# Optimization experiments

Measured on AMD Instinct MI355X. Metric: run time of the kernel, lower is better.

Reference implementation:

```python
import jax, jax.numpy as jnp
import numpy as np

D_MODEL = 1024
K = 256
AMPLITUDE_MAX = 3.0
GATE_BIAS_INIT = 0.65  # alpha-gate bias initialized at logit(0.65)


def setup_inputs() -> dict:
    key = jax.random.key(0)
    k0, k1, k2, k3 = jax.random.split(key, 4)
    B, n = 4, 4096
    x = jax.random.normal(k0, (B, n, D_MODEL), dtype=jnp.float32)
    # OscillatorProjection: Linear(d_model -> 6K), chunks [A, omega, phi, alpha, g, beta]
    W_proj = jax.random.normal(k1, (6 * K, D_MODEL), dtype=jnp.float32) * 0.02
    b_proj = jnp.zeros((6 * K,), dtype=jnp.float32)
    alpha_bias = float(np.log(GATE_BIAS_INIT / (1.0 - GATE_BIAS_INIT)))
    b_proj = b_proj.at[3 * K:4 * K].set(alpha_bias)
    W_res = jax.random.normal(k2, (D_MODEL, 4 * K - 2), dtype=jnp.float32) * 0.002
    W_phase = jax.random.normal(k3, (K, D_MODEL), dtype=jnp.float32) * 0.001
    b_phase = jnp.zeros((K,), dtype=jnp.float32)
    return {
        "x": x, "W_proj": W_proj, "b_proj": b_proj, "W_res": W_res,
        "W_phase": W_phase, "b_phase": b_phase,
        "lambda_pcg": jnp.float32(0.1), "res_scale": jnp.float32(0.05),
    }


def _scan_combine(c1, c2):
    # first-order linear recurrence r_t = a_t * r_{t-1} + b_t (complex, split re/im)
    a1, br1, bi1 = c1
    a2, br2, bi2 = c2
    return (a1 * a2, a2 * br1 + br2, a2 * bi1 + bi2)


def _forward(x, W_proj, b_proj, W_res, W_phase, b_phase, lambda_pcg, res_scale):
    B, n, _ = x.shape
    # OscillatorProjection
    proj = jnp.einsum('bnd,kd->bnk', x, W_proj) + b_proj  # (B, n, 6K)
    a_raw, w_raw, p_raw, al_raw, g_raw, be_raw = jnp.split(proj, 6, axis=-1)
    A = AMPLITUDE_MAX * jax.nn.sigmoid(a_raw)
    omega = jax.nn.softplus(w_raw)
    phi = p_raw
    alpha = jax.nn.sigmoid(al_raw)
    g_out = jax.nn.sigmoid(g_raw)
    beta = jax.nn.sigmoid(be_raw)

    # phase_mode == 'log'
    positions = jnp.log1p(jnp.arange(n, dtype=jnp.float32)).reshape(1, n, 1)
    angle = omega * positions + phi
    cos_a = jnp.cos(angle)
    sin_a = jnp.sin(angle)
    one_m_a = 1.0 - alpha
    drive_r = one_m_a * A * cos_a
    drive_i = one_m_a * A * sin_a

    # parallel associative prefix scan over sequence axis
    _, r_r, r_i = jax.lax.associative_scan(_scan_combine, (alpha, drive_r, drive_i), axis=1)

    # erase (read-and-subtract)
    readout = r_r * cos_a + r_i * sin_a
    r_r = r_r - beta * readout * cos_a
    r_i = r_i - beta * readout * sin_a

    # state norm: r /= max(|r|, 1)
    modulus = jnp.sqrt(r_r * r_r + r_i * r_i + 1e-8)
    scale = jnp.maximum(modulus, 1.0)
    r_r = r_r / scale
    r_i = r_i / scale

    # demodulate: rho = r * exp(-j * angle)
    rho_re = r_r * cos_a + r_i * sin_a
    rho_im = -r_r * sin_a + r_i * cos_a

    # phase-coherence gate
    rho_norm = jnp.sqrt(rho_re * rho_re + rho_im * rho_im + 1e-8)
    phase_query = jnp.einsum('bnd,kd->bnk', x, W_phase) + b_phase
    phase_alignment = (rho_re / rho_norm) * jnp.cos(phase_query) + (rho_im / rho_norm) * jnp.sin(phase_query)
    phase_gate = jax.nn.sigmoid(lambda_pcg * phase_alignment)
    rho_re = phase_gate * rho_re
    rho_im = phase_gate * rho_im

    # SCPM: neighbor complex cross-products
    xcross_re = rho_re[:, :, :-1] * rho_re[:, :, 1:] - rho_im[:, :, :-1] * rho_im[:, :, 1:]
    xcross_im = rho_re[:, :, :-1] * rho_im[:, :, 1:] + rho_im[:, :, :-1] * rho_re[:, :, 1:]
    rho_base = jnp.concatenate([rho_re, rho_im], axis=-1)              # (B, n, 2K)
    g_base = jnp.concatenate([g_out, g_out], axis=-1)
    g_cross = 0.5 * (g_out[:, :, :-1] + g_out[:, :, 1:])
    xcross = jnp.concatenate([xcross_re, xcross_im], axis=-1)          # (B, n, 2K-2)
    g_cross_full = jnp.concatenate([g_cross, g_cross], axis=-1)
    rho = jnp.concatenate([g_base * rho_base, g_cross_full * xcross], axis=-1)  # (B, n, 4K-2)

    # eval mode: warmup_factor == 1.0
    return res_scale * jnp.einsum('bnk,dk->bnd', rho, W_res)


def reference(x, W_proj, b_proj, W_res, W_phase, b_phase, lambda_pcg, res_scale):
    return _forward(x, W_proj, b_proj, W_res, W_phase, b_phase, lambda_pcg, res_scale)
```

## Files before the change

### kernel.cpp

```cpp
#include <hip/hip_runtime.h>
#include <cmath>

#define D_MODEL 1024
#define KOSC    256
#define NSEQ    4096
#define BATCH   4
#define NROW    (BATCH * NSEQ)
#define JTOT    1792

typedef short      s16x8 __attribute__((ext_vector_type(8)));
typedef float      f32x4 __attribute__((ext_vector_type(4)));

#define GL2LDS(gsrc, ldst)                                                      \
  __builtin_amdgcn_global_load_lds(                                             \
      (const __attribute__((address_space(1))) unsigned int*)(gsrc),            \
      (__attribute__((address_space(3))) unsigned int*)(ldst), 16, 0, 0)

__device__ __forceinline__ float sigm(float x) {
    return 1.0f / (1.0f + expf(-x));
}
__device__ __forceinline__ float softplusf_(float x) {
    return fmaxf(x, 0.0f) + log1pf(expf(-fabsf(x)));
}

__device__ __forceinline__ void bf16_split(float f, unsigned short& hi,
                                           unsigned short& lo) {
    unsigned u = __float_as_uint(f);
    unsigned r = u + 0x7FFFu + ((u >> 16) & 1u);
    hi = (unsigned short)(r >> 16);
    float fh = __uint_as_float((unsigned)hi << 16);
    float fl = f - fh;
    unsigned ul = __float_as_uint(fl);
    unsigned rl = ul + 0x7FFFu + ((ul >> 16) & 1u);
    lo = (unsigned short)(rl >> 16);
}

__global__ __launch_bounds__(256) void split_x_kernel(
    const float* __restrict__ x, unsigned short* __restrict__ XH,
    unsigned short* __restrict__ XL)
{
    int i = blockIdx.x * 256 + threadIdx.x;
    float4 v = ((const float4*)x)[i];
    ushort4 h, l;
    bf16_split(v.x, h.x, l.x);
    bf16_split(v.y, h.y, l.y);
    bf16_split(v.z, h.z, l.z);
    bf16_split(v.w, h.w, l.w);
    ((ushort4*)XH)[i] = h;
    ((ushort4*)XL)[i] = l;
}

__global__ __launch_bounds__(256) void split_w_kernel(
    const float* __restrict__ Wproj, const float* __restrict__ Wphase,
    unsigned short* __restrict__ WH, unsigned short* __restrict__ WL)
{
    int i = blockIdx.x * 256 + threadIdx.x;
    int elem = i << 2;
    int row = elem >> 10;
    int col = elem & 1023;
    const float* src = (row < 1536) ? (Wproj + (size_t)row * 1024 + col)
                                    : (Wphase + (size_t)(row - 1536) * 1024 + col);
    float4 v = *(const float4*)src;
    ushort4 h, l;
    bf16_split(v.x, h.x, l.x);
    bf16_split(v.y, h.y, l.y);
    bf16_split(v.z, h.z, l.z);
    bf16_split(v.w, h.w, l.w);
    ((ushort4*)WH)[i] = h;
    ((ushort4*)WL)[i] = l;
}

__global__ __launch_bounds__(256) void pack_wres_kernel(
    const float* __restrict__ Wres, unsigned short* __restrict__ WPH)
{
    int idx = blockIdx.x * 256 + threadIdx.x;
    int d = idx >> 10;
    int j = idx & 1023;
    float v = (j < 1022) ? Wres[(size_t)d * 1022 + j] : 0.0f;
    unsigned u = __float_as_uint(v);
    unsigned r = u + 0x7FFFu + ((u >> 16) & 1u);
    WPH[idx] = (unsigned short)(r >> 16);
}

__global__ __launch_bounds__(256, 3) void gemm1_full_kernel(
    const unsigned short* __restrict__ WH, const unsigned short* __restrict__ WL,
    const unsigned short* __restrict__ XH, const unsigned short* __restrict__ XL,
    const float* __restrict__ bproj, float* __restrict__ PT)
{
    __shared__ __attribute__((aligned(16))) unsigned short AH[4096];
    __shared__ __attribute__((aligned(16))) unsigned short AL[4096];
    __shared__ __attribute__((aligned(16))) unsigned short BH[4096];
    __shared__ __attribute__((aligned(16))) unsigned short BL[4096];

    const int tid  = threadIdx.x;
    const int lane = tid & 63;
    const int w    = tid >> 6;
    const int wm   = w >> 1, wn = w & 1;
    const int m0   = (blockIdx.y + 2) * 128;
    const int n0   = blockIdx.x * 128;
    const int fr   = lane & 15;
    const int fq   = lane >> 4;

    f32x4 acc[4][4];
    #pragma unroll
    for (int i = 0; i < 4; i++)
        #pragma unroll
        for (int j = 0; j < 4; j++) acc[i][j] = (f32x4){0.f, 0.f, 0.f, 0.f};

    for (int kc = 0; kc < 32; kc++) {
        const int kbase = kc * 32;
        __syncthreads();
        #pragma unroll
        for (int t = 0; t < 2; t++) {
            int G  = w * 128 + t * 64 + lane;
            int gm = G & 127;
            int gq = G >> 7;
            size_t offA = (size_t)(m0 + gm) * 1024 + kbase + gq * 8;
            size_t offB = (size_t)(n0 + gm) * 1024 + kbase + gq * 8;
            int ldsg = (w * 128 + t * 64) * 8;
            GL2LDS(WH + offA, &AH[ldsg]);
            GL2LDS(WL + offA, &AL[ldsg]);
            GL2LDS(XH + offB, &BH[ldsg]);
            GL2LDS(XL + offB, &BL[ldsg]);
        }
        __syncthreads();

        s16x8 ah[4], al[4], bh[4], bl[4];
        #pragma unroll
        for (int f = 0; f < 4; f++) {
            int aoff = (fq * 128 + wm * 64 + f * 16 + fr) * 8;
            int boff = (fq * 128 + wn * 64 + f * 16 + fr) * 8;
            ah[f] = *(const s16x8*)&AH[aoff];
            al[f] = *(const s16x8*)&AL[aoff];
            bh[f] = *(const s16x8*)&BH[boff];
            bl[f] = *(const s16x8*)&BL[boff];
        }
        #pragma unroll
        for (int i = 0; i < 4; i++)
            #pragma unroll
            for (int j = 0; j < 4; j++) {
                acc[i][j] = __builtin_amdgcn_mfma_f32_16x16x32_bf16(ah[i], bh[j], acc[i][j], 0, 0, 0);
                acc[i][j] = __builtin_amdgcn_mfma_f32_16x16x32_bf16(ah[i], bl[j], acc[i][j], 0, 0, 0);
                acc[i][j] = __builtin_amdgcn_mfma_f32_16x16x32_bf16(al[i], bh[j], acc[i][j], 0, 0, 0);
            }
    }

    #pragma unroll
    for (int i = 0; i < 4; i++) {
        int mbase = m0 + wm * 64 + i * 16 + fq * 4;
        #pragma unroll
        for (int j = 0; j < 4; j++) {
            int n = n0 + wn * 64 + j * 16 + fr;
            #pragma unroll
            for (int rg = 0; rg < 4; rg++) {
                int m = mbase + rg;
                PT[(size_t)m * NROW + n] = acc[i][j][rg] + bproj[m];
            }
        }
    }
}

__global__ __launch_bounds__(256, 4) void gemm1_lite_kernel(
    const unsigned short* __restrict__ WH, const unsigned short* __restrict__ XH,
    const float* __restrict__ bproj, const float* __restrict__ bphase,
    float* __restrict__ PT)
{
    __shared__ __attribute__((aligned(16))) unsigned short AH[4096];
    __shared__ __attribute__((aligned(16))) unsigned short BH[4096];

    const int tid  = threadIdx.x;
    const int lane = tid & 63;
    const int w    = tid >> 6;
    const int wm   = w >> 1, wn = w & 1;
    const int yt   = blockIdx.y;
    const int jt   = (yt < 2) ? yt : yt + 4;
    const int m0   = jt * 128;
    const int n0   = blockIdx.x * 128;
    const int fr   = lane & 15;
    const int fq   = lane >> 4;

    f32x4 acc[4][4];
    #pragma unroll
    for (int i = 0; i < 4; i++)
        #pragma unroll
        for (int j = 0; j < 4; j++) acc[i][j] = (f32x4){0.f, 0.f, 0.f, 0.f};

    for (int kc = 0; kc < 32; kc++) {
        const int kbase = kc * 32;
        __syncthreads();
        #pragma unroll
        for (int t = 0; t < 2; t++) {
            int G  = w * 128 + t * 64 + lane;
            int gm = G & 127;
            int gq = G >> 7;
            size_t offA = (size_t)(m0 + gm) * 1024 + kbase + gq * 8;
            size_t offB = (size_t)(n0 + gm) * 1024 + kbase + gq * 8;
            int ldsg = (w * 128 + t * 64) * 8;
            GL2LDS(WH + offA, &AH[ldsg]);
            GL2LDS(XH + offB, &BH[ldsg]);
        }
        __syncthreads();

        s16x8 ah[4], bh[4];
        #pragma unroll
        for (int f = 0; f < 4; f++) {
            int aoff = (fq * 128 + wm * 64 + f * 16 + fr) * 8;
            int boff = (fq * 128 + wn * 64 + f * 16 + fr) * 8;
            ah[f] = *(const s16x8*)&AH[aoff];
            bh[f] = *(const s16x8*)&BH[boff];
        }
        #pragma unroll
        for (int i = 0; i < 4; i++)
            #pragma unroll
            for (int j = 0; j < 4; j++)
                acc[i][j] = __builtin_amdgcn_mfma_f32_16x16x32_bf16(ah[i], bh[j], acc[i][j], 0, 0, 0);
    }

    #pragma unroll
    for (int i = 0; i < 4; i++) {
        int mbase = m0 + wm * 64 + i * 16 + fq * 4;
        #pragma unroll
        for (int j = 0; j < 4; j++) {
            int n = n0 + wn * 64 + j * 16 + fr;
            #pragma unroll
            for (int rg = 0; rg < 4; rg++) {
                int m = mbase + rg;
                float bias = (m < 1536) ? bproj[m] : bphase[m - 1536];
                PT[(size_t)m * NROW + n] = acc[i][j][rg] + bias;
            }
        }
    }
}

__global__ __launch_bounds__(256) void scan_kernel(float* PT,
                                                   const float* lambda_ptr)
{
    const int bx = blockIdx.x;
    const int k = bx & 255;
    const int b = bx >> 8;
    const int t = threadIdx.x;
    const size_t colb = (size_t)b * NSEQ;
    const size_t R = NROW;

    float* rowA  = PT + (size_t)(k)        * R + colb;
    float* rowW  = PT + (size_t)(256 + k)  * R + colb;
    float* rowP  = PT + (size_t)(512 + k)  * R + colb;
    float* rowAl = PT + (size_t)(768 + k)  * R + colb;
    float* rowG  = PT + (size_t)(1024 + k) * R + colb;
    float* rowBe = PT + (size_t)(1280 + k) * R + colb;
    float* rowPq = PT + (size_t)(1536 + k) * R + colb;

    __shared__ float s_al[NSEQ + 256];
    __shared__ float s_rr[NSEQ + 256];
    __shared__ float s_ri[NSEQ + 256];
    __shared__ float s_sa[256], s_sbr[256], s_sbi[256];

    const float lam = *lambda_ptr;

    for (int i = 0; i < 16; i++) {
        int n = i * 256 + t;
        float araw = rowA[n];
        float wraw = rowW[n];
        float praw = rowP[n];
        float alraw = rowAl[n];
        float A     = 3.0f * sigm(araw);
        float alpha = sigm(alraw);
        float omega = softplusf_(wraw);
        float ang   = fmaf(omega, log1pf((float)n), praw);
        float sn, cs;
        sincosf(ang, &sn, &cs);
        float amp = (1.0f - alpha) * A;
        int pidx = n + (n >> 4);
        s_al[pidx] = alpha;
        s_rr[pidx] = amp * cs;
        s_ri[pidx] = amp * sn;
    }
    __syncthreads();

    {
        float ap = 1.0f, br = 0.0f, bi = 0.0f;
        int base = t * 17;
        #pragma unroll
        for (int i = 0; i < 16; i++) {
            float a = s_al[base + i];
            br = fmaf(a, br, s_rr[base + i]);
            bi = fmaf(a, bi, s_ri[base + i]);
            ap *= a;
        }
        s_sa[t] = ap; s_sbr[t] = br; s_sbi[t] = bi;
    }
    __syncthreads();

    for (int off = 1; off < 256; off <<= 1) {
        float a2 = s_sa[t], b2r = s_sbr[t], b2i = s_sbi[t];
        float a1 = 1.0f, b1r = 0.0f, b1i = 0.0f;
        if (t >= off) { a1 = s_sa[t - off]; b1r = s_sbr[t - off]; b1i = s_sbi[t - off]; }
        __syncthreads();
        s_sa[t]  = a1 * a2;
        s_sbr[t] = fmaf(a2, b1r, b2r);
        s_sbi[t] = fmaf(a2, b1i, b2i);
        __syncthreads();
    }

    {
        float cr = 0.0f, ci = 0.0f;
        if (t > 0) { cr = s_sbr[t - 1]; ci = s_sbi[t - 1]; }
        int base = t * 17;
        #pragma unroll
        for (int i = 0; i < 16; i++) {
            float a = s_al[base + i];
            cr = fmaf(a, cr, s_rr[base + i]);
            ci = fmaf(a, ci, s_ri[base + i]);
            s_rr[base + i] = cr;
            s_ri[base + i] = ci;
        }
    }
    __syncthreads();

    for (int i = 0; i < 16; i++) {
        int n = i * 256 + t;
        float wraw = rowW[n];
        float praw = rowP[n];
        float beraw = rowBe[n];
        float graw = rowG[n];
        float pq = rowPq[n];

        float omega = softplusf_(wraw);
        float ang = fmaf(omega, log1pf((float)n), praw);
        float sn, cs;
        sincosf(ang, &sn, &cs);

        int pidx = n + (n >> 4);
        float rr = s_rr[pidx], ri = s_ri[pidx];
        float beta = sigm(beraw);
        float g = sigm(graw);

        float readout = rr * cs + ri * sn;
        rr -= beta * readout * cs;
        ri -= beta * readout * sn;

        float modulus = sqrtf(rr * rr + ri * ri + 1e-8f);
        float scale = fmaxf(modulus, 1.0f);
        rr /= scale; ri /= scale;

        float rho_re = rr * cs + ri * sn;
        float rho_im = -rr * sn + ri * cs;

        float rho_norm = sqrtf(rho_re * rho_re + rho_im * rho_im + 1e-8f);
        float sq, cq;
        sincosf(pq, &sq, &cq);
        float pa = (rho_re * cq + rho_im * sq) / rho_norm;
        float gate = sigm(lam * pa);
        rho_re *= gate;
        rho_im *= gate;

        rowA[n] = rho_re;
        rowW[n] = rho_im;
        rowP[n] = g;
    }
}

__global__ __launch_bounds__(256) void pack_rho_kernel(
    const float* __restrict__ PT, unsigned short* __restrict__ RTH,
    unsigned short* __restrict__ RTL)
{
    __shared__ float s_re[256 * 33];
    __shared__ float s_im[256 * 33];
    __shared__ float s_g [256 * 33];

    const int tid = threadIdx.x;
    const int r0 = blockIdx.x * 32;

    {
        int lr = tid & 31;
        int k0 = tid >> 5;
        for (int it = 0; it < 32; it++) {
            int k = it * 8 + k0;
            size_t go = (size_t)k * NROW + r0 + lr;
            s_re[k * 33 + lr] = PT[go];
            s_im[k * 33 + lr] = PT[(size_t)256 * NROW + go];
            s_g [k * 33 + lr] = PT[(size_t)512 * NROW + go];
        }
    }
    __syncthreads();

    const int r = tid >> 3;
    const int c = tid & 7;
    for (int i = 0; i < 16; i++) {
        int jb = (c + 8 * i) * 8;
        unsigned short h[8], l[8];
        #pragma unroll
        for (int e = 0; e < 8; e++) {
            int j = jb + e;
            float v;
            if (j < 256) {
                v = s_g[j * 33 + r] * s_re[j * 33 + r];
            } else if (j < 512) {
                int k = j - 256;
                v = s_g[k * 33 + r] * s_im[k * 33 + r];
            } else if (j < 767) {
                int k = j - 512;
                float gc = 0.5f * (s_g[k * 33 + r] + s_g[(k + 1) * 33 + r]);
                v = gc * (s_re[k * 33 + r] * s_re[(k + 1) * 33 + r]
                        - s_im[k * 33 + r] * s_im[(k + 1) * 33 + r]);
            } else if (j < 1022) {
                int k = j - 767;
                float gc = 0.5f * (s_g[k * 33 + r] + s_g[(k + 1) * 33 + r]);
                v = gc * (s_re[k * 33 + r] * s_im[(k + 1) * 33 + r]
                        + s_im[k * 33 + r] * s_re[(k + 1) * 33 + r]);
            } else {
                v = 0.0f;
            }
            bf16_split(v, h[e], l[e]);
        }
        size_t off = (size_t)(r0 + r) * 1024 + jb;
        s16x8 hv, lv;
        #pragma unroll
        for (int e = 0; e < 8; e++) { hv[e] = (short)h[e]; lv[e] = (short)l[e]; }
        *(s16x8*)&RTH[off] = hv;
        *(s16x8*)&RTL[off] = lv;
    }
}

__global__ __launch_bounds__(256, 3) void gemm2_kernel(
    const unsigned short* __restrict__ WPH,
    const unsigned short* __restrict__ RTH, const unsigned short* __restrict__ RTL,
    const float* __restrict__ rs_ptr, float* __restrict__ out)
{
    __shared__ __attribute__((aligned(16))) unsigned short AH[4096];
    __shared__ __attribute__((aligned(16))) unsigned short BH[4096];
    __shared__ __attribute__((aligned(16))) unsigned short BL[4096];

    const int tid  = threadIdx.x;
    const int lane = tid & 63;
    const int w    = tid >> 6;
    const int wm   = w >> 1, wn = w & 1;
    const int m0   = blockIdx.y * 128;
    const int n0   = blockIdx.x * 128;
    const int fr   = lane & 15;
    const int fq   = lane >> 4;
    const float rs = *rs_ptr;

    f32x4 acc[4][4];
    #pragma unroll
    for (int i = 0; i < 4; i++)
        #pragma unroll
        for (int j = 0; j < 4; j++) acc[i][j] = (f32x4){0.f, 0.f, 0.f, 0.f};

    for (int kc = 0; kc < 32; kc++) {
        const int kbase = kc * 32;
        __syncthreads();
        #pragma unroll
        for (int t = 0; t < 2; t++) {
            int G  = w * 128 + t * 64 + lane;
            int gm = G & 127;
            int gq = G >> 7;
            size_t offA = (size_t)(m0 + gm) * 1024 + kbase + gq * 8;
            size_t offB = (size_t)(n0 + gm) * 1024 + kbase + gq * 8;
            int ldsg = (w * 128 + t * 64) * 8;
            GL2LDS(WPH + offA, &AH[ldsg]);
            GL2LDS(RTH + offB, &BH[ldsg]);
            GL2LDS(RTL + offB, &BL[ldsg]);
        }
        __syncthreads();

        s16x8 ah[4], bh[4], bl[4];
        #pragma unroll
        for (int f = 0; f < 4; f++) {
            int aoff = (fq * 128 + wm * 64 + f * 16 + fr) * 8;
            int boff = (fq * 128 + wn * 64 + f * 16 + fr) * 8;
            ah[f] = *(const s16x8*)&AH[aoff];
            bh[f] = *(const s16x8*)&BH[boff];
            bl[f] = *(const s16x8*)&BL[boff];
        }
        #pragma unroll
        for (int i = 0; i < 4; i++)
            #pragma unroll
            for (int j = 0; j < 4; j++) {
                acc[i][j] = __builtin_amdgcn_mfma_f32_16x16x32_bf16(ah[i], bh[j], acc[i][j], 0, 0, 0);
                acc[i][j] = __builtin_amdgcn_mfma_f32_16x16x32_bf16(ah[i], bl[j], acc[i][j], 0, 0, 0);
            }
    }

    #pragma unroll
    for (int i = 0; i < 4; i++) {
        int d = m0 + wm * 64 + i * 16 + fq * 4;
        #pragma unroll
        for (int j = 0; j < 4; j++) {
            int n = n0 + wn * 64 + j * 16 + fr;
            float4 v = { rs * acc[i][j][0], rs * acc[i][j][1],
                         rs * acc[i][j][2], rs * acc[i][j][3] };
            *(float4*)&out[(size_t)n * 1024 + d] = v;
        }
    }
}

extern "C" void kernel_launch(void* const* d_in, const int* in_sizes, int n_in,
                              void* d_out, int out_size, void* d_ws, size_t ws_size,
                              hipStream_t stream)
{
    const float* x      = (const float*)d_in[0];
    const float* Wproj  = (const float*)d_in[1];
    const float* bproj  = (const float*)d_in[2];
    const float* Wres   = (const float*)d_in[3];
    const float* Wphase = (const float*)d_in[4];
    const float* bphase = (const float*)d_in[5];
    const float* lam    = (const float*)d_in[6];
    const float* rs     = (const float*)d_in[7];
    float* out = (float*)d_out;

    float* PT = (float*)d_ws;
    unsigned short* WH  = (unsigned short*)((char*)d_ws + (size_t)JTOT * NROW * 4);
    unsigned short* WL  = WH + (size_t)JTOT * 1024;
    unsigned short* RTH = (unsigned short*)(PT + (size_t)768 * NROW);
    unsigned short* RTL = RTH + (size_t)NROW * 1024;
    unsigned short* WPH = (unsigned short*)PT;
    unsigned short* XH  = (unsigned short*)d_out;
    unsigned short* XL  = XH + (size_t)NROW * 1024;

    hipLaunchKernelGGL(split_x_kernel, dim3(NROW * D_MODEL / 1024), dim3(256), 0, stream,
                       x, XH, XL);
    hipLaunchKernelGGL(split_w_kernel, dim3(JTOT * D_MODEL / 1024), dim3(256), 0, stream,
                       Wproj, Wphase, WH, WL);
    hipLaunchKernelGGL(gemm1_full_kernel, dim3(NROW / 128, 4), dim3(256), 0, stream,
                       WH, WL, XH, XL, bproj, PT);
    hipLaunchKernelGGL(gemm1_lite_kernel, dim3(NROW / 128, 10), dim3(256), 0, stream,
                       WH, XH, bproj, bphase, PT);
    hipLaunchKernelGGL(scan_kernel, dim3(BATCH * KOSC), dim3(256), 0, stream,
                       PT, lam);
    hipLaunchKernelGGL(pack_rho_kernel, dim3(NROW / 32), dim3(256), 0, stream,
                       PT, RTH, RTL);
    hipLaunchKernelGGL(pack_wres_kernel, dim3(1024 * 1024 / 256), dim3(256), 0, stream,
                       Wres, WPH);
    hipLaunchKernelGGL(gemm2_kernel, dim3(NROW / 128, 1024 / 128), dim3(256), 0, stream,
                       WPH, RTH, RTL, rs, out);
}
```

Measured before the change: 535.1 us.

## Unify GEMMs into double-buffered 256x256 tile core with merged gemm1 launch

Replaces the 128x128 single-buffered GEMM kernels with a shared templated 256x256-tile core run by 512 threads. The core double-buffers LDS, prefetching the next K chunk while MFMAs run, and raises wave priority during compute. The full-precision and lite gemm1 launches become one kernel that picks the precision path per row tile, and gemm2 uses the same core. The aims are more reuse per tile, hidden global-load latency and fewer launches, at the cost of more registers and LDS per block, lower occupancy, and fewer blocks for the GPU to schedule.

```diff
diff --git a/kernel.cpp b/kernel.cpp
--- a/kernel.cpp
+++ b/kernel.cpp
@@ -82,150 +82,151 @@
     WPH[idx] = (unsigned short)(r >> 16);
 }
 
-__global__ __launch_bounds__(256, 3) void gemm1_full_kernel(
-    const unsigned short* __restrict__ WH, const unsigned short* __restrict__ WL,
-    const unsigned short* __restrict__ XH, const unsigned short* __restrict__ XL,
-    const float* __restrict__ bproj, float* __restrict__ PT)
-{
-    __shared__ __attribute__((aligned(16))) unsigned short AH[4096];
-    __shared__ __attribute__((aligned(16))) unsigned short AL[4096];
-    __shared__ __attribute__((aligned(16))) unsigned short BH[4096];
-    __shared__ __attribute__((aligned(16))) unsigned short BL[4096];
-
+template<int NKS, int HAS_AL, int HAS_BL>
+__device__ __forceinline__ void gemm256_core(
+    const unsigned short* __restrict__ gAH, const unsigned short* __restrict__ gAL,
+    const unsigned short* __restrict__ gBH, const unsigned short* __restrict__ gBL,
+    unsigned short* sAH, unsigned short* sAL,
+    unsigned short* sBH, unsigned short* sBL,
+    int m0, int n0, f32x4 (&acc)[8][4])
+{
     const int tid  = threadIdx.x;
     const int lane = tid & 63;
     const int w    = tid >> 6;
-    const int wm   = w >> 1, wn = w & 1;
-    const int m0   = (blockIdx.y + 2) * 128;
-    const int n0   = blockIdx.x * 128;
+    const int wm   = w >> 2;
+    const int wn   = w & 3;
     const int fr   = lane & 15;
     const int fq   = lane >> 4;
-
-    f32x4 acc[4][4];
+    const int BK   = 32 * NKS;
+    const int BUFS = 256 * BK;
+    const int NKT  = 1024 / BK;
+
+    auto stage = [&](int buf, int kc, int t) {
+        const int G   = t * 512 + tid;
+        const int row = G & 255;
+        const int q   = G >> 8;
+        const size_t ka   = (size_t)kc * BK + q * 8;
+        const size_t offA = (size_t)(m0 + row) * 1024 + ka;
+        const size_t offB = (size_t)(n0 + row) * 1024 + ka;
+        const int ldso = buf * BUFS + (t * 512 + w * 64) * 8;
+        GL2LDS(gAH + offA, &sAH[ldso]);
+        if (HAS_AL) GL2LDS(gAL + offA, &sAL[ldso]);
+        GL2LDS(gBH + offB, &sBH[ldso]);
+        if (HAS_BL) GL2LDS(gBL + offB, &sBL[ldso]);
+    };
+
     #pragma unroll
-    for (int i = 0; i < 4; i++)
+    for (int t = 0; t < 2 * NKS; t++) stage(0, 0, t);
+
+    for (int kc = 0; kc < NKT; kc++) {
+        const int cur   = kc & 1;
+        const int cbase = cur * BUFS;
+        asm volatile("s_waitcnt vmcnt(0)" ::: "memory");
+        __builtin_amdgcn_s_barrier();
+
+        #pragma unroll
+        for (int p = 0; p < 4; p++) {
+            const int qi = p & 1;
+            const int qj = p >> 1;
+
+            s16x8 fah[4][NKS], fal[4][NKS], fbh[2][NKS], fbl[2][NKS];
+            #pragma unroll
+            for (int ii = 0; ii < 4; ii++) {
+                const int i = qi * 4 + ii;
+                #pragma unroll
+                for (int s = 0; s < NKS; s++) {
+                    const int off = cbase +
+                        (((s * 4 + fq) * 256 + wm * 128 + i * 16 + fr) * 8);
+                    fah[ii][s] = *(const s16x8*)&sAH[off];
+                    if (HAS_AL) fal[ii][s] = *(const s16x8*)&sAL[off];
+                }
+            }
+            #pragma unroll
+            for (int jj = 0; jj < 2; jj++) {
+                const int j = qj * 2 + jj;
+                #pragma unroll
+                for (int s = 0; s < NKS; s++) {
+                    const int off = cbase +
+                        (((s * 4 + fq) * 256 + wn * 64 + j * 16 + fr) * 8);
+                    fbh[jj][s] = *(const s16x8*)&sBH[off];
+                    if (HAS_BL) fbl[jj][s] = *(const s16x8*)&sBL[off];
+                }
+            }
+
+            if (p < 2 && kc + 1 < NKT) {
+                #pragma unroll
+                for (int t = 0; t < NKS; t++)
+                    stage(cur ^ 1, kc + 1, p * NKS + t);
+            }
+
+            __builtin_amdgcn_s_barrier();
+            __builtin_amdgcn_s_setprio(1);
+            #pragma unroll
+            for (int ii = 0; ii < 4; ii++) {
+                #pragma unroll
+                for (int jj = 0; jj < 2; jj++) {
+                    const int i = qi * 4 + ii;
+                    const int j = qj * 2 + jj;
+                    #pragma unroll
+                    for (int s = 0; s < NKS; s++) {
+                        acc[i][j] = __builtin_amdgcn_mfma_f32_16x16x32_bf16(
+                            fah[ii][s], fbh[jj][s], acc[i][j], 0, 0, 0);
+                        if (HAS_BL)
+                            acc[i][j] = __builtin_amdgcn_mfma_f32_16x16x32_bf16(
+                                fah[ii][s], fbl[jj][s], acc[i][j], 0, 0, 0);
+                        if (HAS_AL)
+                            acc[i][j] = __builtin_amdgcn_mfma_f32_16x16x32_bf16(
+                                fal[ii][s], fbh[jj][s], acc[i][j], 0, 0, 0);
+                    }
+                }
+            }
+            __builtin_amdgcn_s_setprio(0);
+            if (p < 3) __builtin_amdgcn_s_barrier();
+        }
+    }
+}
+
+__global__ __launch_bounds__(512, 2) void gemm1_kernel(
+    const unsigned short* __restrict__ WH, const unsigned short* __restrict__ WL,
+    const unsigned short* __restrict__ XH, const unsigned short* __restrict__ XL,
+    const float* __restrict__ bproj, const float* __restrict__ bphase,
+    float* __restrict__ PT)
+{
+    __shared__ __attribute__((aligned(16))) unsigned short smem[65536];
+    const int yt = blockIdx.y;
+    const int m0 = yt * 256;
+    const int n0 = blockIdx.x * 256;
+
+    f32x4 acc[8][4];
+    #pragma unroll
+    for (int i = 0; i < 8; i++)
         #pragma unroll
         for (int j = 0; j < 4; j++) acc[i][j] = (f32x4){0.f, 0.f, 0.f, 0.f};
 
-    for (int kc = 0; kc < 32; kc++) {
-        const int kbase = kc * 32;
-        __syncthreads();
-        #pragma unroll
-        for (int t = 0; t < 2; t++) {
-            int G  = w * 128 + t * 64 + lane;
-            int gm = G & 127;
-            int gq = G >> 7;
-            size_t offA = (size_t)(m0 + gm) * 1024 + kbase + gq * 8;
-            size_t offB = (size_t)(n0 + gm) * 1024 + kbase + gq * 8;
-            int ldsg = (w * 128 + t * 64) * 8;
-            GL2LDS(WH + offA, &AH[ldsg]);
-            GL2LDS(WL + offA, &AL[ldsg]);
-            GL2LDS(XH + offB, &BH[ldsg]);
-            GL2LDS(XL + offB, &BL[ldsg]);
-        }
-        __syncthreads();
-
-        s16x8 ah[4], al[4], bh[4], bl[4];
-        #pragma unroll
-        for (int f = 0; f < 4; f++) {
-            int aoff = (fq * 128 + wm * 64 + f * 16 + fr) * 8;
-            int boff = (fq * 128 + wn * 64 + f * 16 + fr) * 8;
-            ah[f] = *(const s16x8*)&AH[aoff];
-            al[f] = *(const s16x8*)&AL[aoff];
-            bh[f] = *(const s16x8*)&BH[boff];
-            bl[f] = *(const s16x8*)&BL[boff];
-        }
-        #pragma unroll
-        for (int i = 0; i < 4; i++)
-            #pragma unroll
-            for (int j = 0; j < 4; j++) {
-                acc[i][j] = __builtin_amdgcn_mfma_f32_16x16x32_bf16(ah[i], bh[j], acc[i][j], 0, 0, 0);
-                acc[i][j] = __builtin_amdgcn_mfma_f32_16x16x32_bf16(ah[i], bl[j], acc[i][j], 0, 0, 0);
-                acc[i][j] = __builtin_amdgcn_mfma_f32_16x16x32_bf16(al[i], bh[j], acc[i][j], 0, 0, 0);
-            }
-    }
-
+    if (yt == 1 || yt == 2) {
+        gemm256_core<1, 1, 1>(WH, WL, XH, XL,
+                              smem, smem + 16384, smem + 32768, smem + 49152,
+                              m0, n0, acc);
+    } else {
+        gemm256_core<2, 0, 0>(WH, nullptr, XH, nullptr,
+                              smem, nullptr, smem + 32768, nullptr,
+                              m0, n0, acc);
+    }
+
+    const int lane = threadIdx.x & 63;
+    const int w    = threadIdx.x >> 6;
+    const int wm   = w >> 2, wn = w & 3;
+    const int fr   = lane & 15, fq = lane >> 4;
     #pragma unroll
-    for (int i = 0; i < 4; i++) {
-        int mbase = m0 + wm * 64 + i * 16 + fq * 4;
+    for (int i = 0; i < 8; i++) {
+        const int mb = m0 + wm * 128 + i * 16 + fq * 4;
         #pragma unroll
         for (int j = 0; j < 4; j++) {
-            int n = n0 + wn * 64 + j * 16 + fr;
+            const int n = n0 + wn * 64 + j * 16 + fr;
             #pragma unroll
             for (int rg = 0; rg < 4; rg++) {
-                int m = mbase + rg;
-                PT[(size_t)m * NROW + n] = acc[i][j][rg] + bproj[m];
-            }
-        }
-    }
-}
-
-__global__ __launch_bounds__(256, 4) void gemm1_lite_kernel(
-    const unsigned short* __restrict__ WH, const unsigned short* __restrict__ XH,
-    const float* __restrict__ bproj, const float* __restrict__ bphase,
-    float* __restrict__ PT)
-{
-    __shared__ __attribute__((aligned(16))) unsigned short AH[4096];
-    __shared__ __attribute__((aligned(16))) unsigned short BH[4096];
-
-    const int tid  = threadIdx.x;
-    const int lane = tid & 63;
-    const int w    = tid >> 6;
-    const int wm   = w >> 1, wn = w & 1;
-    const int yt   = blockIdx.y;
-    const int jt   = (yt < 2) ? yt : yt + 4;
-    const int m0   = jt * 128;
-    const int n0   = blockIdx.x * 128;
-    const int fr   = lane & 15;
-    const int fq   = lane >> 4;
-
-    f32x4 acc[4][4];
-    #pragma unroll
-    for (int i = 0; i < 4; i++)
-        #pragma unroll
-        for (int j = 0; j < 4; j++) acc[i][j] = (f32x4){0.f, 0.f, 0.f, 0.f};
-
-    for (int kc = 0; kc < 32; kc++) {
-        const int kbase = kc * 32;
-        __syncthreads();
-        #pragma unroll
-        for (int t = 0; t < 2; t++) {
-            int G  = w * 128 + t * 64 + lane;
-            int gm = G & 127;
-            int gq = G >> 7;
-            size_t offA = (size_t)(m0 + gm) * 1024 + kbase + gq * 8;
-            size_t offB = (size_t)(n0 + gm) * 1024 + kbase + gq * 8;
-            int ldsg = (w * 128 + t * 64) * 8;
-            GL2LDS(WH + offA, &AH[ldsg]);
-            GL2LDS(XH + offB, &BH[ldsg]);
-        }
-        __syncthreads();
-
-        s16x8 ah[4], bh[4];
-        #pragma unroll
-        for (int f = 0; f < 4; f++) {
-            int aoff = (fq * 128 + wm * 64 + f * 16 + fr) * 8;
-            int boff = (fq * 128 + wn * 64 + f * 16 + fr) * 8;
-            ah[f] = *(const s16x8*)&AH[aoff];
-            bh[f] = *(const s16x8*)&BH[boff];
-        }
-        #pragma unroll
-        for (int i = 0; i < 4; i++)
-            #pragma unroll
-            for (int j = 0; j < 4; j++)
-                acc[i][j] = __builtin_amdgcn_mfma_f32_16x16x32_bf16(ah[i], bh[j], acc[i][j], 0, 0, 0);
-    }
-
-    #pragma unroll
-    for (int i = 0; i < 4; i++) {
-        int mbase = m0 + wm * 64 + i * 16 + fq * 4;
-        #pragma unroll
-        for (int j = 0; j < 4; j++) {
-            int n = n0 + wn * 64 + j * 16 + fr;
-            #pragma unroll
-            for (int rg = 0; rg < 4; rg++) {
-                int m = mbase + rg;
-                float bias = (m < 1536) ? bproj[m] : bphase[m - 1536];
+                const int m = mb + rg;
+                const float bias = (m < 1536) ? bproj[m] : bphase[m - 1536];
                 PT[(size_t)m * NROW + n] = acc[i][j][rg] + bias;
             }
         }
@@ -422,72 +423,36 @@
     }
 }
 
-__global__ __launch_bounds__(256, 3) void gemm2_kernel(
+__global__ __launch_bounds__(512, 2) void gemm2_kernel(
     const unsigned short* __restrict__ WPH,
     const unsigned short* __restrict__ RTH, const unsigned short* __restrict__ RTL,
     const float* __restrict__ rs_ptr, float* __restrict__ out)
 {
-    __shared__ __attribute__((aligned(16))) unsigned short AH[4096];
-    __shared__ __attribute__((aligned(16))) unsigned short BH[4096];
-    __shared__ __attribute__((aligned(16))) unsigned short BL[4096];
-
-    const int tid  = threadIdx.x;
-    const int lane = tid & 63;
-    const int w    = tid >> 6;
-    const int wm   = w >> 1, wn = w & 1;
-    const int m0   = blockIdx.y * 128;
-    const int n0   = blockIdx.x * 128;
-    const int fr   = lane & 15;
-    const int fq   = lane >> 4;
+    __shared__ __attribute__((aligned(16))) unsigned short smem[49152];
+    const int m0 = blockIdx.y * 256;
+    const int n0 = blockIdx.x * 256;
     const float rs = *rs_ptr;
 
-    f32x4 acc[4][4];
+    f32x4 acc[8][4];
     #pragma unroll
-    for (int i = 0; i < 4; i++)
+    for (int i = 0; i < 8; i++)
         #pragma unroll
         for (int j = 0; j < 4; j++) acc[i][j] = (f32x4){0.f, 0.f, 0.f, 0.f};
 
-    for (int kc = 0; kc < 32; kc++) {
-        const int kbase = kc * 32;
-        __syncthreads();
-        #pragma unroll
-        for (int t = 0; t < 2; t++) {
-            int G  = w * 128 + t * 64 + lane;
-            int gm = G & 127;
-            int gq = G >> 7;
-            size_t offA = (size_t)(m0 + gm) * 1024 + kbase + gq * 8;
-            size_t offB = (size_t)(n0 + gm) * 1024 + kbase + gq * 8;
-            int ldsg = (w * 128 + t * 64) * 8;
-            GL2LDS(WPH + offA, &AH[ldsg]);
-            GL2LDS(RTH + offB, &BH[ldsg]);
-            GL2LDS(RTL + offB, &BL[ldsg]);
-        }
-        __syncthreads();
-
-        s16x8 ah[4], bh[4], bl[4];
-        #pragma unroll
-        for (int f = 0; f < 4; f++) {
-            int aoff = (fq * 128 + wm * 64 + f * 16 + fr) * 8;
-            int boff = (fq * 128 + wn * 64 + f * 16 + fr) * 8;
-            ah[f] = *(const s16x8*)&AH[aoff];
-            bh[f] = *(const s16x8*)&BH[boff];
-            bl[f] = *(const s16x8*)&BL[boff];
-        }
-        #pragma unroll
-        for (int i = 0; i < 4; i++)
-            #pragma unroll
-            for (int j = 0; j < 4; j++) {
-                acc[i][j] = __builtin_amdgcn_mfma_f32_16x16x32_bf16(ah[i], bh[j], acc[i][j], 0, 0, 0);
-                acc[i][j] = __builtin_amdgcn_mfma_f32_16x16x32_bf16(ah[i], bl[j], acc[i][j], 0, 0, 0);
-            }
-    }
-
+    gemm256_core<1, 0, 1>(WPH, nullptr, RTH, RTL,
+                          smem, nullptr, smem + 16384, smem + 32768,
+                          m0, n0, acc);
+
+    const int lane = threadIdx.x & 63;
+    const int w    = threadIdx.x >> 6;
+    const int wm   = w >> 2, wn = w & 3;
+    const int fr   = lane & 15, fq = lane >> 4;
     #pragma unroll
-    for (int i = 0; i < 4; i++) {
-        int d = m0 + wm * 64 + i * 16 + fq * 4;
+    for (int i = 0; i < 8; i++) {
+        const int d = m0 + wm * 128 + i * 16 + fq * 4;
         #pragma unroll
         for (int j = 0; j < 4; j++) {
-            int n = n0 + wn * 64 + j * 16 + fr;
+            const int n = n0 + wn * 64 + j * 16 + fr;
             float4 v = { rs * acc[i][j][0], rs * acc[i][j][1],
                          rs * acc[i][j][2], rs * acc[i][j][3] };
             *(float4*)&out[(size_t)n * 1024 + d] = v;
@@ -522,16 +487,14 @@
                        x, XH, XL);
     hipLaunchKernelGGL(split_w_kernel, dim3(JTOT * D_MODEL / 1024), dim3(256), 0, stream,
                        Wproj, Wphase, WH, WL);
-    hipLaunchKernelGGL(gemm1_full_kernel, dim3(NROW / 128, 4), dim3(256), 0, stream,
-                       WH, WL, XH, XL, bproj, PT);
-    hipLaunchKernelGGL(gemm1_lite_kernel, dim3(NROW / 128, 10), dim3(256), 0, stream,
-                       WH, XH, bproj, bphase, PT);
+    hipLaunchKernelGGL(gemm1_kernel, dim3(NROW / 256, 7), dim3(512), 0, stream,
+                       WH, WL, XH, XL, bproj, bphase, PT);
     hipLaunchKernelGGL(scan_kernel, dim3(BATCH * KOSC), dim3(256), 0, stream,
                        PT, lam);
     hipLaunchKernelGGL(pack_rho_kernel, dim3(NROW / 32), dim3(256), 0, stream,
                        PT, RTH, RTL);
     hipLaunchKernelGGL(pack_wres_kernel, dim3(1024 * 1024 / 256), dim3(256), 0, stream,
                        Wres, WPH);
-    hipLaunchKernelGGL(gemm2_kernel, dim3(NROW / 128, 1024 / 128), dim3(256), 0, stream,
+    hipLaunchKernelGGL(gemm2_kernel, dim3(NROW / 256, 1024 / 256), dim3(512), 0, stream,
                        WPH, RTH, RTL, rs, out);
 }
```

Result: slower. 582.5 us (+8.9%).
